# Kernel tuning notes

Hardware: AMD Instinct MI355X
Metric: run time of the kernel (lower is better)

Reference implementation:

```python
import jax, jax.numpy as jnp
import numpy as np

B, N, C1, C2, H = 4, 4096, 320, 256, 5
HD = C1 // H  # 64


def setup_inputs() -> dict:
    key = jax.random.key(0)
    ks = jax.random.split(key, 9)
    w = lambda k, shape, fan_in: jax.random.normal(k, shape, jnp.float32) * (fan_in ** -0.5)
    return {
        "x1": jax.random.normal(ks[0], (B, N, C1), jnp.float32),
        "x2": jax.random.normal(ks[1], (B, N, C2), jnp.float32),
        # nn.Linear weights, torch layout [out_features, in_features]
        "q1_w": w(ks[2], (C1, C1), C1),
        "q2_w": w(ks[3], (C1, C2), C2),
        "kv1_w": w(ks[4], (2 * C1, C2), C2),
        "kv2_w": w(ks[5], (2 * C1, C1), C1),
        "proj1_w": w(ks[6], (C1, C1), C1),
        "proj1_b": jnp.zeros((C1,), jnp.float32),
        "proj2_w": w(ks[7], (C1, C1), C1),
        "proj2_b": jnp.zeros((C1,), jnp.float32),
    }


def _branch(xq, xkv, q_w, kv_w, proj_w, proj_b):
    b, n, _ = xq.shape
    scale = HD ** -0.5
    q = (xq @ q_w.T).reshape(b, n, H, HD).transpose(0, 2, 1, 3)          # [B,H,N,HD]
    kv = (xkv @ kv_w.T).reshape(b, n, 2, H, HD).transpose(2, 0, 3, 1, 4)  # [2,B,H,N,HD]
    k, v = kv[0], kv[1]
    attn = jax.nn.softmax(jnp.einsum('bhqd,bhkd->bhqk', q * scale, k), axis=-1)
    y = jnp.einsum('bhqk,bhkd->bhqd', attn, v)                            # [B,H,N,HD]
    y = y.transpose(0, 2, 1, 3).reshape(b, n, C1)
    return y @ proj_w.T + proj_b


def reference(x1, x2, q1_w, q2_w, kv1_w, kv2_w, proj1_w, proj1_b, proj2_w, proj2_b):
    y1 = _branch(x1, x2, q1_w, kv1_w, proj1_w, proj1_b)  # x1 queries, x2 keys/values
    y2 = _branch(x2, x1, q2_w, kv2_w, proj2_w, proj2_b)  # x2 queries, x1 keys/values
    return jnp.concatenate((y1, y2), axis=-1)            # [B,N,2*C1]
```

## Files before the change

kernel.cpp:

```cpp
#include <hip/hip_runtime.h>
#include <hip/hip_bf16.h>

#define Bb 4
#define Nn 4096
#define C1 320
#define C2 256
#define Hh 5
#define HD 64
#define Mm (Bb*Nn)

using bf16 = __hip_bfloat16;
typedef __attribute__((ext_vector_type(8))) short  short8;
typedef __attribute__((ext_vector_type(4))) short  short4_;
typedef __attribute__((ext_vector_type(4))) float  f32x4;

__device__ __forceinline__ short f2s(float f) {
    bf16 h = __float2bfloat16(f);
    short s;
    __builtin_memcpy(&s, &h, 2);
    return s;
}

__device__ __forceinline__ float fexp2(float x) {
#if __has_builtin(__builtin_amdgcn_exp2f)
    return __builtin_amdgcn_exp2f(x);
#else
    return exp2f(x);
#endif
}

__device__ __forceinline__ int swz(int row, int bb) {
    return row * 64 + ((bb ^ (row & 7)) << 3);
}

struct CvtArgs {
    const float* s[8];
    bf16* d[8];
    int off[9];
};

__global__ void cvt_all(CvtArgs a) {
    int i = (blockIdx.x * blockDim.x + threadIdx.x) * 4;
    if (i >= a.off[8]) return;
    int seg = 0;
    #pragma unroll
    for (int k = 1; k < 8; ++k) seg += (i >= a.off[k]);
    int j = i - a.off[seg];
    float4 v = *(const float4*)(a.s[seg] + j);
    short4_ o = { f2s(v.x), f2s(v.y), f2s(v.z), f2s(v.w) };
    *(short4_*)(a.d[seg] + j) = o;
}

__global__ __launch_bounds__(256) void gemm_bt(
    const bf16* __restrict__ A, const bf16* __restrict__ W,
    int K, int mode, float oscale,
    bf16* __restrict__ O1, bf16* __restrict__ O2,
    const float* __restrict__ bias, float* __restrict__ Of, int ooff)
{
    __shared__ bf16 la[64 * 64];
    __shared__ bf16 lw[64 * 64];
    const int m0 = blockIdx.x * 64, n0 = blockIdx.y * 64;
    const int t = threadIdx.x;
    const int wave = t >> 6, lane = t & 63, l16 = lane & 15, quad = lane >> 4;
    const int sr = t >> 3, sb = t & 7;

    f32x4 acc[4] = {{0.f,0.f,0.f,0.f},{0.f,0.f,0.f,0.f},{0.f,0.f,0.f,0.f},{0.f,0.f,0.f,0.f}};

    const int nk = K >> 6;
    short8 ra0 = *(const short8*)(A + (size_t)(m0 + sr) * K + sb * 8);
    short8 ra1 = *(const short8*)(A + (size_t)(m0 + sr + 32) * K + sb * 8);
    short8 rw0 = *(const short8*)(W + (size_t)(n0 + sr) * K + sb * 8);
    short8 rw1 = *(const short8*)(W + (size_t)(n0 + sr + 32) * K + sb * 8);

    for (int kt = 0; kt < nk; ++kt) {
        __syncthreads();
        *(short8*)&la[swz(sr, sb)]      = ra0;
        *(short8*)&la[swz(sr + 32, sb)] = ra1;
        *(short8*)&lw[swz(sr, sb)]      = rw0;
        *(short8*)&lw[swz(sr + 32, sb)] = rw1;
        __syncthreads();
        if (kt + 1 < nk) {
            const int k0 = (kt + 1) * 64;
            ra0 = *(const short8*)(A + (size_t)(m0 + sr) * K + k0 + sb * 8);
            ra1 = *(const short8*)(A + (size_t)(m0 + sr + 32) * K + k0 + sb * 8);
            rw0 = *(const short8*)(W + (size_t)(n0 + sr) * K + k0 + sb * 8);
            rw1 = *(const short8*)(W + (size_t)(n0 + sr + 32) * K + k0 + sb * 8);
        }
        const int arow = wave * 16 + l16;
        short8 a0 = *(const short8*)&la[swz(arow, quad)];
        short8 a1 = *(const short8*)&la[swz(arow, quad + 4)];
        #pragma unroll
        for (int nt = 0; nt < 4; ++nt) {
            const int brow = nt * 16 + l16;
            short8 b0 = *(const short8*)&lw[swz(brow, quad)];
            short8 b1 = *(const short8*)&lw[swz(brow, quad + 4)];
            acc[nt] = __builtin_amdgcn_mfma_f32_16x16x32_bf16(a0, b0, acc[nt], 0, 0, 0);
            acc[nt] = __builtin_amdgcn_mfma_f32_16x16x32_bf16(a1, b1, acc[nt], 0, 0, 0);
        }
    }

    const int mrow = m0 + wave * 16 + quad * 4;
    if (mode == 2) {
        #pragma unroll
        for (int nt = 0; nt < 4; ++nt) {
            int col = n0 + nt * 16 + l16;
            float bv = bias[col];
            #pragma unroll
            for (int r = 0; r < 4; ++r)
                Of[(size_t)(mrow + r) * 640 + ooff + col] = acc[nt][r] + bv;
        }
    } else if (mode == 0 || n0 < C1) {
        #pragma unroll
        for (int nt = 0; nt < 4; ++nt) {
            int col = n0 + nt * 16 + l16;
            #pragma unroll
            for (int r = 0; r < 4; ++r)
                O1[(size_t)(mrow + r) * C1 + col] = __float2bfloat16(acc[nt][r] * oscale);
        }
    } else {
        #pragma unroll
        for (int nt = 0; nt < 4; ++nt) {
            int col = n0 + nt * 16 + l16 - C1;
            int h = col >> 6, d = col & 63;
            #pragma unroll
            for (int r = 0; r < 4; ++r) {
                int m = mrow + r;
                int b = m >> 12, n = m & (Nn - 1);
                O2[((size_t)(b * Hh + h) * 64 + d) * Nn + n] = __float2bfloat16(acc[nt][r]);
            }
        }
    }
}

__global__ __launch_bounds__(256) void flash_kernel(
    const bf16* __restrict__ Q1, const bf16* __restrict__ K1,
    const bf16* __restrict__ V1, bf16* __restrict__ Y1,
    const bf16* __restrict__ Q2, const bf16* __restrict__ K2,
    const bf16* __restrict__ V2, bf16* __restrict__ Y2)
{
    __shared__ bf16 lk[64 * 64];
    __shared__ bf16 lv[64 * 64];
    __shared__ bf16 lp[4 * 32 * 64];
    const int qt = blockIdx.x, h = blockIdx.y, z = blockIdx.z;
    const int b = z & 3, branch = z >> 2;
    const bf16* Q  = branch ? Q2 : Q1;
    const bf16* Km = branch ? K2 : K1;
    const bf16* Vt = branch ? V2 : V1;
    bf16*       Y  = branch ? Y2 : Y1;

    const int t = threadIdx.x;
    const int wave = t >> 6, lane = t & 63, l16 = lane & 15, quad = lane >> 4;
    const int sr = t >> 3, sb = t & 7;

    short8 aq[2][2];
    #pragma unroll
    for (int qf = 0; qf < 2; ++qf) {
        const bf16* qptr = Q + (size_t)(b * Nn + qt * 128 + wave * 32 + qf * 16 + l16) * C1
                             + h * HD + quad * 8;
        aq[qf][0] = *(const short8*)qptr;
        aq[qf][1] = *(const short8*)(qptr + 32);
    }

    f32x4 acc[2][4];
    #pragma unroll
    for (int qf = 0; qf < 2; ++qf)
        #pragma unroll
        for (int i = 0; i < 4; ++i) acc[qf][i] = {0.f,0.f,0.f,0.f};
    float lsum[2] = {0.f, 0.f};

    const bf16* Kbase = Km + (size_t)b * Nn * C1 + h * HD;
    const bf16* Vbase = Vt + (size_t)(b * Hh + h) * 64 * Nn;
    const int wbase = wave * (32 * 64);

    short8 rk0 = *(const short8*)(Kbase + (size_t)sr * C1 + sb * 8);
    short8 rk1 = *(const short8*)(Kbase + (size_t)(sr + 32) * C1 + sb * 8);
    short8 rv0 = *(const short8*)(Vbase + (size_t)sr * Nn + sb * 8);
    short8 rv1 = *(const short8*)(Vbase + (size_t)(sr + 32) * Nn + sb * 8);

    const int NT = Nn / 64;
    for (int kt = 0; kt < NT; ++kt) {
        __syncthreads();
        *(short8*)&lk[swz(sr, sb)]      = rk0;
        *(short8*)&lk[swz(sr + 32, sb)] = rk1;
        *(short8*)&lv[swz(sr, sb)]      = rv0;
        *(short8*)&lv[swz(sr + 32, sb)] = rv1;
        __syncthreads();
        if (kt + 1 < NT) {
            const int kn = (kt + 1) * 64;
            rk0 = *(const short8*)(Kbase + (size_t)(kn + sr) * C1 + sb * 8);
            rk1 = *(const short8*)(Kbase + (size_t)(kn + sr + 32) * C1 + sb * 8);
            rv0 = *(const short8*)(Vbase + (size_t)sr * Nn + kn + sb * 8);
            rv1 = *(const short8*)(Vbase + (size_t)(sr + 32) * Nn + kn + sb * 8);
        }

        #pragma unroll
        for (int nt = 0; nt < 4; ++nt) {
            const int krow = nt * 16 + l16;
            short8 k0 = *(const short8*)&lk[swz(krow, quad)];
            short8 k1 = *(const short8*)&lk[swz(krow, quad + 4)];
            #pragma unroll
            for (int qf = 0; qf < 2; ++qf) {
                f32x4 z4 = {0.f, 0.f, 0.f, 0.f};
                z4 = __builtin_amdgcn_mfma_f32_16x16x32_bf16(k0, aq[qf][0], z4, 0, 0, 0);
                z4 = __builtin_amdgcn_mfma_f32_16x16x32_bf16(k1, aq[qf][1], z4, 0, 0, 0);
                float p0 = fexp2(z4[0]);
                float p1 = fexp2(z4[1]);
                float p2 = fexp2(z4[2]);
                float p3 = fexp2(z4[3]);
                lsum[qf] += (p0 + p1) + (p2 + p3);
                short4_ pk = { f2s(p0), f2s(p1), f2s(p2), f2s(p3) };
                const int prow = qf * 16 + l16;
                *(short4_*)&lp[wbase + swz(prow, nt * 2 + (quad >> 1)) + (quad & 1) * 4] = pk;
            }
        }

        short8 ap[2][2];
        #pragma unroll
        for (int qf = 0; qf < 2; ++qf) {
            const int prow = qf * 16 + l16;
            ap[qf][0] = *(const short8*)&lp[wbase + swz(prow, quad)];
            ap[qf][1] = *(const short8*)&lp[wbase + swz(prow, quad + 4)];
        }
        #pragma unroll
        for (int dt = 0; dt < 4; ++dt) {
            const int vrow = dt * 16 + l16;
            short8 bv0 = *(const short8*)&lv[swz(vrow, quad)];
            short8 bv1 = *(const short8*)&lv[swz(vrow, quad + 4)];
            #pragma unroll
            for (int qf = 0; qf < 2; ++qf) {
                acc[qf][dt] = __builtin_amdgcn_mfma_f32_16x16x32_bf16(ap[qf][0], bv0, acc[qf][dt], 0, 0, 0);
                acc[qf][dt] = __builtin_amdgcn_mfma_f32_16x16x32_bf16(ap[qf][1], bv1, acc[qf][dt], 0, 0, 0);
            }
        }
    }

    #pragma unroll
    for (int qf = 0; qf < 2; ++qf) {
        float l = lsum[qf];
        l += __shfl_xor(l, 16, 64);
        l += __shfl_xor(l, 32, 64);
        #pragma unroll
        for (int reg = 0; reg < 4; ++reg) {
            float lr = __shfl(l, quad * 4 + reg, 64);
            float inv = 1.0f / lr;
            size_t rowoff = (size_t)(b * Nn + qt * 128 + wave * 32 + qf * 16 + quad * 4 + reg) * C1
                          + h * HD + l16;
            #pragma unroll
            for (int dt = 0; dt < 4; ++dt)
                Y[rowoff + dt * 16] = __float2bfloat16(acc[qf][dt][reg] * inv);
        }
    }
}

extern "C" void kernel_launch(void* const* d_in, const int* in_sizes, int n_in,
                              void* d_out, int out_size, void* d_ws, size_t ws_size,
                              hipStream_t stream)
{
    const float* x1   = (const float*)d_in[0];
    const float* x2   = (const float*)d_in[1];
    const float* q1w  = (const float*)d_in[2];
    const float* q2w  = (const float*)d_in[3];
    const float* kv1w = (const float*)d_in[4];
    const float* kv2w = (const float*)d_in[5];
    const float* p1w  = (const float*)d_in[6];
    const float* p1b  = (const float*)d_in[7];
    const float* p2w  = (const float*)d_in[8];
    const float* p2b  = (const float*)d_in[9];
    float* out = (float*)d_out;

    bf16* ws = (bf16*)d_ws;
    size_t o = 0;
    bf16* x1b  = ws + o; o += (size_t)Mm * C1;
    bf16* x2b  = ws + o; o += (size_t)Mm * C2;
    bf16* wq1  = ws + o; o += C1 * C1;
    bf16* wq2  = ws + o; o += C1 * C2;
    bf16* wkv1 = ws + o; o += 2 * C1 * C2;
    bf16* wkv2 = ws + o; o += 2 * C1 * C1;
    bf16* wp1  = ws + o; o += C1 * C1;
    bf16* wp2  = ws + o; o += C1 * C1;
    bf16* Q1   = ws + o; o += (size_t)Mm * C1;
    bf16* K1   = ws + o; o += (size_t)Mm * C1;
    bf16* V1t  = ws + o; o += (size_t)Mm * C1;
    bf16* Q2   = ws + o; o += (size_t)Mm * C1;
    bf16* K2   = ws + o; o += (size_t)Mm * C1;
    bf16* V2t  = ws + o; o += (size_t)Mm * C1;
    bf16* Y1   = ws + o; o += (size_t)Mm * C1;
    bf16* Y2   = ws + o; o += (size_t)Mm * C1;
    (void)ws_size; (void)in_sizes; (void)n_in; (void)out_size;

    CvtArgs ca;
    ca.s[0] = x1;   ca.d[0] = x1b;  int n0 = Mm * C1;
    ca.s[1] = x2;   ca.d[1] = x2b;  int n1 = Mm * C2;
    ca.s[2] = q1w;  ca.d[2] = wq1;  int n2 = C1 * C1;
    ca.s[3] = q2w;  ca.d[3] = wq2;  int n3 = C1 * C2;
    ca.s[4] = kv1w; ca.d[4] = wkv1; int n4 = 2 * C1 * C2;
    ca.s[5] = kv2w; ca.d[5] = wkv2; int n5 = 2 * C1 * C1;
    ca.s[6] = p1w;  ca.d[6] = wp1;  int n6 = C1 * C1;
    ca.s[7] = p2w;  ca.d[7] = wp2;  int n7 = C1 * C1;
    int ns[8] = {n0, n1, n2, n3, n4, n5, n6, n7};
    ca.off[0] = 0;
    for (int i = 0; i < 8; ++i) ca.off[i + 1] = ca.off[i] + ns[i];
    int total = ca.off[8];
    cvt_all<<<dim3((total / 4 + 255) / 256), 256, 0, stream>>>(ca);

    const float QS = 0.125f * 1.4426950408889634f;

    gemm_bt<<<dim3(Mm / 64, C1 / 64), 256, 0, stream>>>(x1b, wq1, C1, 0, QS, Q1, nullptr, nullptr, nullptr, 0);
    gemm_bt<<<dim3(Mm / 64, (2 * C1) / 64), 256, 0, stream>>>(x2b, wkv1, C2, 1, 1.0f, K1, V1t, nullptr, nullptr, 0);
    gemm_bt<<<dim3(Mm / 64, C1 / 64), 256, 0, stream>>>(x2b, wq2, C2, 0, QS, Q2, nullptr, nullptr, nullptr, 0);
    gemm_bt<<<dim3(Mm / 64, (2 * C1) / 64), 256, 0, stream>>>(x1b, wkv2, C1, 1, 1.0f, K2, V2t, nullptr, nullptr, 0);

    flash_kernel<<<dim3(Nn / 128, Hh, 2 * Bb), 256, 0, stream>>>(Q1, K1, V1t, Y1, Q2, K2, V2t, Y2);

    gemm_bt<<<dim3(Mm / 64, C1 / 64), 256, 0, stream>>>(Y1, wp1, C1, 2, 1.0f, nullptr, nullptr, p1b, out, 0);
    gemm_bt<<<dim3(Mm / 64, C1 / 64), 256, 0, stream>>>(Y2, wp2, C1, 2, 1.0f, nullptr, nullptr, p2b, out, C1);
}
```

Measured before the change: 371.9 us.

## Rewrite flash attention with 32x32 MFMA and register-resident P via permlane swap

```diff
diff --git a/kernel.cpp b/kernel.cpp
--- a/kernel.cpp
+++ b/kernel.cpp
@@ -13,6 +13,7 @@
 typedef __attribute__((ext_vector_type(8))) short  short8;
 typedef __attribute__((ext_vector_type(4))) short  short4_;
 typedef __attribute__((ext_vector_type(4))) float  f32x4;
+typedef __attribute__((ext_vector_type(16))) float f32x16;
 
 __device__ __forceinline__ short f2s(float f) {
     bf16 h = __float2bfloat16(f);
@@ -31,6 +32,27 @@
 
 __device__ __forceinline__ int swz(int row, int bb) {
     return row * 64 + ((bb ^ (row & 7)) << 3);
+}
+
+__device__ __forceinline__ unsigned cvtpk(float lo, float hi) {
+    unsigned r;
+    asm("v_cvt_pk_bf16_f32 %0, %1, %2" : "=v"(r) : "v"(lo), "v"(hi));
+    return r;
+}
+
+__device__ __forceinline__ void plswap(unsigned &a, unsigned &b) {
+#if __has_builtin(__builtin_amdgcn_permlane32_swap)
+    auto r = __builtin_amdgcn_permlane32_swap(a, b, false, false);
+    a = r[0]; b = r[1];
+#else
+    asm("v_permlane32_swap_b32 %0, %1" : "+v"(a), "+v"(b));
+#endif
+}
+
+__device__ __forceinline__ short8 mk8(unsigned d0, unsigned d1, unsigned d2, unsigned d3) {
+    union { unsigned u[4]; short8 s; } u;
+    u.u[0] = d0; u.u[1] = d1; u.u[2] = d2; u.u[3] = d3;
+    return u.s;
 }
 
 struct CvtArgs {
@@ -132,7 +154,7 @@
     }
 }
 
-__global__ __launch_bounds__(256) void flash_kernel(
+__global__ __launch_bounds__(256, 2) void flash_kernel(
     const bf16* __restrict__ Q1, const bf16* __restrict__ K1,
     const bf16* __restrict__ V1, bf16* __restrict__ Y1,
     const bf16* __restrict__ Q2, const bf16* __restrict__ K2,
@@ -140,37 +162,39 @@
 {
     __shared__ bf16 lk[64 * 64];
     __shared__ bf16 lv[64 * 64];
-    __shared__ bf16 lp[4 * 32 * 64];
     const int qt = blockIdx.x, h = blockIdx.y, z = blockIdx.z;
     const int b = z & 3, branch = z >> 2;
     const bf16* Q  = branch ? Q2 : Q1;
     const bf16* Km = branch ? K2 : K1;
     const bf16* Vt = branch ? V2 : V1;
-    bf16*       Y  = branch ? Y2 : Y1;
+    bf16*       Yo = branch ? Y2 : Y1;
 
     const int t = threadIdx.x;
-    const int wave = t >> 6, lane = t & 63, l16 = lane & 15, quad = lane >> 4;
+    const int wave = t >> 6, lane = t & 63;
+    const int l32 = lane & 31, hi = lane >> 5;
     const int sr = t >> 3, sb = t & 7;
 
-    short8 aq[2][2];
+    const int qrow0 = qt * 256 + wave * 64;
+
+    short8 qf[2][4];
     #pragma unroll
-    for (int qf = 0; qf < 2; ++qf) {
-        const bf16* qptr = Q + (size_t)(b * Nn + qt * 128 + wave * 32 + qf * 16 + l16) * C1
-                             + h * HD + quad * 8;
-        aq[qf][0] = *(const short8*)qptr;
-        aq[qf][1] = *(const short8*)(qptr + 32);
-    }
-
-    f32x4 acc[2][4];
+    for (int qb = 0; qb < 2; ++qb) {
+        const bf16* qptr = Q + (size_t)(b * Nn + qrow0 + qb * 32 + l32) * C1 + h * HD + hi * 8;
+        #pragma unroll
+        for (int ksd = 0; ksd < 4; ++ksd)
+            qf[qb][ksd] = *(const short8*)(qptr + ksd * 16);
+    }
+
+    f32x16 o[2][2];
     #pragma unroll
-    for (int qf = 0; qf < 2; ++qf)
-        #pragma unroll
-        for (int i = 0; i < 4; ++i) acc[qf][i] = {0.f,0.f,0.f,0.f};
+    for (int qb = 0; qb < 2; ++qb)
+        #pragma unroll
+        for (int db = 0; db < 2; ++db)
+            o[qb][db] = (f32x16){0.f,0.f,0.f,0.f,0.f,0.f,0.f,0.f,0.f,0.f,0.f,0.f,0.f,0.f,0.f,0.f};
     float lsum[2] = {0.f, 0.f};
 
     const bf16* Kbase = Km + (size_t)b * Nn * C1 + h * HD;
     const bf16* Vbase = Vt + (size_t)(b * Hh + h) * 64 * Nn;
-    const int wbase = wave * (32 * 64);
 
     short8 rk0 = *(const short8*)(Kbase + (size_t)sr * C1 + sb * 8);
     short8 rk1 = *(const short8*)(Kbase + (size_t)(sr + 32) * C1 + sb * 8);
@@ -194,60 +218,60 @@
         }
 
         #pragma unroll
-        for (int nt = 0; nt < 4; ++nt) {
-            const int krow = nt * 16 + l16;
-            short8 k0 = *(const short8*)&lk[swz(krow, quad)];
-            short8 k1 = *(const short8*)&lk[swz(krow, quad + 4)];
-            #pragma unroll
-            for (int qf = 0; qf < 2; ++qf) {
-                f32x4 z4 = {0.f, 0.f, 0.f, 0.f};
-                z4 = __builtin_amdgcn_mfma_f32_16x16x32_bf16(k0, aq[qf][0], z4, 0, 0, 0);
-                z4 = __builtin_amdgcn_mfma_f32_16x16x32_bf16(k1, aq[qf][1], z4, 0, 0, 0);
-                float p0 = fexp2(z4[0]);
-                float p1 = fexp2(z4[1]);
-                float p2 = fexp2(z4[2]);
-                float p3 = fexp2(z4[3]);
-                lsum[qf] += (p0 + p1) + (p2 + p3);
-                short4_ pk = { f2s(p0), f2s(p1), f2s(p2), f2s(p3) };
-                const int prow = qf * 16 + l16;
-                *(short4_*)&lp[wbase + swz(prow, nt * 2 + (quad >> 1)) + (quad & 1) * 4] = pk;
+        for (int kb = 0; kb < 2; ++kb) {
+            short8 ka[4];
+            #pragma unroll
+            for (int ksd = 0; ksd < 4; ++ksd)
+                ka[ksd] = *(const short8*)&lk[swz(kb * 32 + l32, ksd * 2 + hi)];
+
+            short8 pa[2][2];
+            #pragma unroll
+            for (int qb = 0; qb < 2; ++qb) {
+                f32x16 s = (f32x16){0.f,0.f,0.f,0.f,0.f,0.f,0.f,0.f,0.f,0.f,0.f,0.f,0.f,0.f,0.f,0.f};
+                #pragma unroll
+                for (int ksd = 0; ksd < 4; ++ksd)
+                    s = __builtin_amdgcn_mfma_f32_32x32x16_bf16(ka[ksd], qf[qb][ksd], s, 0, 0, 0);
+                float p[16];
+                #pragma unroll
+                for (int r = 0; r < 16; ++r) p[r] = fexp2(s[r]);
+                lsum[qb] += (((p[0]+p[1])+(p[2]+p[3])) + ((p[4]+p[5])+(p[6]+p[7])))
+                          + (((p[8]+p[9])+(p[10]+p[11])) + ((p[12]+p[13])+(p[14]+p[15])));
+                unsigned d0 = cvtpk(p[0],  p[1]),  d2 = cvtpk(p[4],  p[5]);
+                plswap(d0, d2);
+                unsigned d1 = cvtpk(p[2],  p[3]),  d3 = cvtpk(p[6],  p[7]);
+                plswap(d1, d3);
+                pa[qb][0] = mk8(d0, d1, d2, d3);
+                unsigned e0 = cvtpk(p[8],  p[9]),  e2 = cvtpk(p[12], p[13]);
+                plswap(e0, e2);
+                unsigned e1 = cvtpk(p[10], p[11]), e3 = cvtpk(p[14], p[15]);
+                plswap(e1, e3);
+                pa[qb][1] = mk8(e0, e1, e2, e3);
             }
-        }
-
-        short8 ap[2][2];
-        #pragma unroll
-        for (int qf = 0; qf < 2; ++qf) {
-            const int prow = qf * 16 + l16;
-            ap[qf][0] = *(const short8*)&lp[wbase + swz(prow, quad)];
-            ap[qf][1] = *(const short8*)&lp[wbase + swz(prow, quad + 4)];
-        }
-        #pragma unroll
-        for (int dt = 0; dt < 4; ++dt) {
-            const int vrow = dt * 16 + l16;
-            short8 bv0 = *(const short8*)&lv[swz(vrow, quad)];
-            short8 bv1 = *(const short8*)&lv[swz(vrow, quad + 4)];
-            #pragma unroll
-            for (int qf = 0; qf < 2; ++qf) {
-                acc[qf][dt] = __builtin_amdgcn_mfma_f32_16x16x32_bf16(ap[qf][0], bv0, acc[qf][dt], 0, 0, 0);
-                acc[qf][dt] = __builtin_amdgcn_mfma_f32_16x16x32_bf16(ap[qf][1], bv1, acc[qf][dt], 0, 0, 0);
+
+            #pragma unroll
+            for (int ks = 0; ks < 2; ++ks) {
+                #pragma unroll
+                for (int db = 0; db < 2; ++db) {
+                    short8 bv = *(const short8*)&lv[swz(db * 32 + l32, kb * 4 + ks * 2 + hi)];
+                    o[0][db] = __builtin_amdgcn_mfma_f32_32x32x16_bf16(pa[0][ks], bv, o[0][db], 0, 0, 0);
+                    o[1][db] = __builtin_amdgcn_mfma_f32_32x32x16_bf16(pa[1][ks], bv, o[1][db], 0, 0, 0);
+                }
             }
         }
     }
 
     #pragma unroll
-    for (int qf = 0; qf < 2; ++qf) {
-        float l = lsum[qf];
-        l += __shfl_xor(l, 16, 64);
-        l += __shfl_xor(l, 32, 64);
-        #pragma unroll
-        for (int reg = 0; reg < 4; ++reg) {
-            float lr = __shfl(l, quad * 4 + reg, 64);
-            float inv = 1.0f / lr;
-            size_t rowoff = (size_t)(b * Nn + qt * 128 + wave * 32 + qf * 16 + quad * 4 + reg) * C1
-                          + h * HD + l16;
-            #pragma unroll
-            for (int dt = 0; dt < 4; ++dt)
-                Y[rowoff + dt * 16] = __float2bfloat16(acc[qf][dt][reg] * inv);
+    for (int qb = 0; qb < 2; ++qb) {
+        float l = lsum[qb] + __shfl_xor(lsum[qb], 32, 64);
+        float inv = 1.0f / l;
+        #pragma unroll
+        for (int r = 0; r < 16; ++r) {
+            const int qr = (r & 3) + 8 * (r >> 2) + 4 * hi;
+            float invr = __shfl(inv, qr, 64);
+            size_t row = (size_t)(b * Nn + qrow0 + qb * 32 + qr);
+            #pragma unroll
+            for (int db = 0; db < 2; ++db)
+                Yo[row * C1 + h * HD + db * 32 + l32] = __float2bfloat16(o[qb][db][r] * invr);
         }
     }
 }
@@ -310,7 +334,7 @@
     gemm_bt<<<dim3(Mm / 64, C1 / 64), 256, 0, stream>>>(x2b, wq2, C2, 0, QS, Q2, nullptr, nullptr, nullptr, 0);
     gemm_bt<<<dim3(Mm / 64, (2 * C1) / 64), 256, 0, stream>>>(x1b, wkv2, C1, 1, 1.0f, K2, V2t, nullptr, nullptr, 0);
 
-    flash_kernel<<<dim3(Nn / 128, Hh, 2 * Bb), 256, 0, stream>>>(Q1, K1, V1t, Y1, Q2, K2, V2t, Y2);
+    flash_kernel<<<dim3(Nn / 256, Hh, 2 * Bb), 256, 0, stream>>>(Q1, K1, V1t, Y1, Q2, K2, V2t, Y2);
 
     gemm_bt<<<dim3(Mm / 64, C1 / 64), 256, 0, stream>>>(Y1, wp1, C1, 2, 1.0f, nullptr, nullptr, p1b, out, 0);
     gemm_bt<<<dim3(Mm / 64, C1 / 64), 256, 0, stream>>>(Y2, wp2, C1, 2, 1.0f, nullptr, nullptr, p2b, out, C1);
```

Result: faster. 351.6 us (-5.5%).
